# Performance work log

Hardware: AMD Instinct MI355X
Metric: run time of the kernel (lower is better)

## Reference

```python
import jax, jax.numpy as jnp
import numpy as np

D_MODEL = 1024
D_FF = 4096


def _layernorm(x, g, b, eps=1e-5):
    mu = jnp.mean(x, axis=-1, keepdims=True)
    var = jnp.var(x, axis=-1, keepdims=True)
    return (x - mu) * jax.lax.rsqrt(var + eps) * g + b


def setup_inputs() -> dict:
    key = jax.random.key(0)
    ks = jax.random.split(key, 16)
    d, f = D_MODEL, D_FF
    s = 1.0 / np.sqrt(d)
    inp = {
        'x': jax.random.normal(ks[0], (4, 2048, d), dtype=jnp.float32),
        'wq': jax.random.uniform(ks[1], (d, d), jnp.float32, -s, s),
        'bq': jax.random.uniform(ks[2], (d,), jnp.float32, -s, s),
        'wk': jax.random.uniform(ks[3], (d, d), jnp.float32, -s, s),
        'bk': jax.random.uniform(ks[4], (d,), jnp.float32, -s, s),
        'wv': jax.random.uniform(ks[5], (d, d), jnp.float32, -s, s),
        'bv': jax.random.uniform(ks[6], (d,), jnp.float32, -s, s),
        'wo': jax.random.uniform(ks[7], (d, d), jnp.float32, -s, s),
        'bo': jax.random.uniform(ks[8], (d,), jnp.float32, -s, s),
        'w1': jax.random.uniform(ks[9], (d, f), jnp.float32, -s, s),
        'b1': jax.random.uniform(ks[10], (f,), jnp.float32, -s, s),
        'w2': jax.random.uniform(ks[11], (f, d), jnp.float32, -1.0 / np.sqrt(f), 1.0 / np.sqrt(f)),
        'b2': jax.random.uniform(ks[12], (d,), jnp.float32, -1.0 / np.sqrt(f), 1.0 / np.sqrt(f)),
        'g1': jnp.ones((d,), jnp.float32),
        'be1': jnp.zeros((d,), jnp.float32),
        'g2': jnp.ones((d,), jnp.float32),
        'be2': jnp.zeros((d,), jnp.float32),
    }
    return inp


def reference(x, wq, bq, wk, bk, wv, bv, wo, bo, w1, b1, w2, b2, g1, be1, g2, be2):
    d_k = x.shape[-1]
    q = jnp.einsum('bsd,de->bse', x, wq) + bq
    k = jnp.einsum('bsd,de->bse', x, wk) + bk
    v = jnp.einsum('bsd,de->bse', x, wv) + bv
    # full-width attention (no head split in the original module)
    scores = jnp.einsum('bqd,bkd->bqk', q, k) / jnp.sqrt(jnp.float32(d_k))
    attn = jax.nn.softmax(scores, axis=-1)
    ctx = jnp.einsum('bqk,bkd->bqd', attn, v)
    attn_out = jnp.einsum('bsd,de->bse', ctx, wo) + bo
    x1 = _layernorm(x + attn_out, g1, be1)
    ff = jnp.einsum('bsf,fd->bsd', jax.nn.relu(jnp.einsum('bsd,df->bsf', x1, w1) + b1), w2) + b2
    return _layernorm(x1 + ff, g2, be2)
```

## Files before the change

kernel.cpp:

```cpp
#include <hip/hip_runtime.h>
#include <stdint.h>


using f32x4 = __attribute__((ext_vector_type(4))) float;
using s16x8 = __attribute__((ext_vector_type(8))) short;

__device__ __forceinline__ ushort f2b(float f) {
    union { float f; uint32_t u; } v; v.f = f;
    uint32_t u = v.u;
    return (ushort)((u + 0x7fffu + ((u >> 16) & 1u)) >> 16);
}
__device__ __forceinline__ float b2f(ushort b) {
    union { uint32_t u; float f; } v; v.u = ((uint32_t)b) << 16;
    return v.f;
}
__device__ __forceinline__ float to_f(float f) { return f; }
__device__ __forceinline__ float to_f(ushort b) { return b2f(b); }

__device__ __forceinline__ void async_ld16(const ushort* g, ushort* l) {
    __builtin_amdgcn_global_load_lds(
        (const __attribute__((address_space(1))) void*)g,
        (__attribute__((address_space(3))) void*)l,
        16, 0, 0);
}


__global__ __launch_bounds__(256) void cast_f2b4(const float* __restrict__ src,
                                                 ushort* __restrict__ dst,
                                                 long long n4) {
    long long i = (long long)blockIdx.x * 256 + threadIdx.x;
    if (i >= n4) return;
    float4 f = ((const float4*)src)[i];
    ushort4 o;
    o.x = f2b(f.x); o.y = f2b(f.y); o.z = f2b(f.z); o.w = f2b(f.w);
    ((ushort4*)dst)[i] = o;
}


template <typename T>
__global__ __launch_bounds__(256) void transpose_to_bf16(const T* __restrict__ src,
                                                         ushort* __restrict__ dst,
                                                         int R, int C, int srcLd,
                                                         long long ss, long long ds) {
    __shared__ float tile[32][33];
    src += (long long)blockIdx.z * ss;
    dst += (long long)blockIdx.z * ds;
    const int c0 = blockIdx.x * 32;
    const int r0 = blockIdx.y * 32;
    const int tx = threadIdx.x, ty = threadIdx.y;
#pragma unroll
    for (int i = 0; i < 4; i++) {
        int r = r0 + ty + i * 8;
        tile[ty + i * 8][tx] = to_f(src[(long long)r * srcLd + c0 + tx]);
    }
    __syncthreads();
#pragma unroll
    for (int i = 0; i < 4; i++) {
        int r = c0 + ty + i * 8;
        dst[(long long)r * R + r0 + tx] = f2b(tile[tx][ty + i * 8]);
    }
}


#define BM 128
#define BN 128
#define BKK 32

template <int OUT_BF16, int RELU, int HAS_BIAS>
__global__ __launch_bounds__(256) void gemm_bt(const ushort* __restrict__ A,
                                               const ushort* __restrict__ BT,
                                               void* __restrict__ Cp,
                                               const float* __restrict__ bias,
                                               int N, int K, int kChunks, float scale,
                                               int lda, int ldb, int ldc,
                                               long long sA, long long sB, long long sC,
                                               long long sK) {
    __shared__ ushort As[BM * BKK];
    __shared__ ushort Bs[BN * BKK];

    const int tid = threadIdx.x;
    const int kIdx = blockIdx.z % kChunks;
    const int bz = blockIdx.z / kChunks;
    const int kLen = K / kChunks;
    const int kOff = kIdx * kLen;
    const ushort* Ab = A + (long long)bz * sA;
    const ushort* Bb = BT + (long long)bz * sB;

    const int W = gridDim.x, H = gridDim.y;
    const int b = blockIdx.y * W + blockIdx.x;
    const int Hp = H >> 3;
    const int xcd = b & 7;
    const int s = b >> 3;
    const int tn = s / Hp;
    const int tm = xcd * Hp + (s % Hp);

    const int lane = tid & 63;
    const int wave = tid >> 6;
    const int wm = (wave >> 1) * 64;
    const int wn = (wave & 1) * 64;
    const int quad = lane >> 4;
    const int l16 = lane & 15;

    const int srow = wave * 32 + (lane >> 2);
    const int scol = (lane & 3) * 8;
    const ushort* AgL = Ab + (long long)(tm * BM + srow) * lda + scol + kOff;
    const ushort* BgL = Bb + (long long)(tn * BN + srow) * ldb + scol + kOff;
    ushort* AsL = As + wave * 1024;
    ushort* BsL = Bs + wave * 1024;
    const long long rstepA = (long long)16 * lda;
    const long long rstepB = (long long)16 * ldb;

    f32x4 acc[4][4];
#pragma unroll
    for (int i = 0; i < 4; i++)
#pragma unroll
        for (int j = 0; j < 4; j++) acc[i][j] = (f32x4){0.f, 0.f, 0.f, 0.f};

    for (int k0 = 0; k0 < kLen; k0 += BKK) {
        async_ld16(AgL + k0, AsL);
        async_ld16(AgL + rstepA + k0, AsL + 512);
        async_ld16(BgL + k0, BsL);
        async_ld16(BgL + rstepB + k0, BsL + 512);
        __syncthreads();

        s16x8 af[4], bf[4];
#pragma unroll
        for (int i = 0; i < 4; i++)
            af[i] = *(const s16x8*)&As[(wm + i * 16 + l16) * BKK + quad * 8];
#pragma unroll
        for (int j = 0; j < 4; j++)
            bf[j] = *(const s16x8*)&Bs[(wn + j * 16 + l16) * BKK + quad * 8];
#pragma unroll
        for (int i = 0; i < 4; i++)
#pragma unroll
            for (int j = 0; j < 4; j++)
                acc[i][j] = __builtin_amdgcn_mfma_f32_16x16x32_bf16(af[i], bf[j], acc[i][j], 0, 0, 0);
        __syncthreads();
    }

    const long long cb = (long long)bz * sC + (long long)kIdx * sK;
    float* Cf = (float*)Cp;
    ushort* Cb = (ushort*)Cp;
#pragma unroll
    for (int j = 0; j < 4; j++) {
        const int col = tn * BN + wn + j * 16 + l16;
        float bv = (HAS_BIAS && kIdx == 0) ? bias[col] : 0.0f;
#pragma unroll
        for (int i = 0; i < 4; i++) {
            const int row0 = tm * BM + wm + i * 16 + quad * 4;
#pragma unroll
            for (int r = 0; r < 4; r++) {
                float v = acc[i][j][r] * scale + bv;
                if (RELU) v = v > 0.f ? v : 0.f;
                long long idx = cb + (long long)(row0 + r) * ldc + col;
                if (OUT_BF16) Cb[idx] = f2b(v);
                else Cf[idx] = v;
            }
        }
    }
}


__global__ __launch_bounds__(256) void softmax_rows(const float* __restrict__ S,
                                                    ushort* __restrict__ P) {
    const int C = 2048;
    const long long row = blockIdx.x;
    const float* s = S + row * C;
    ushort* p = P + row * C;
    const int tid = threadIdx.x;
    float v[8];
    float mx = -1e30f;
#pragma unroll
    for (int i = 0; i < 8; i++) {
        v[i] = s[tid + i * 256];
        mx = fmaxf(mx, v[i]);
    }
    __shared__ float red[256];
    red[tid] = mx;
    __syncthreads();
    for (int off = 128; off > 0; off >>= 1) {
        if (tid < off) red[tid] = fmaxf(red[tid], red[tid + off]);
        __syncthreads();
    }
    mx = red[0];
    __syncthreads();
    float sum = 0.f;
#pragma unroll
    for (int i = 0; i < 8; i++) {
        v[i] = __expf(v[i] - mx);
        sum += v[i];
    }
    red[tid] = sum;
    __syncthreads();
    for (int off = 128; off > 0; off >>= 1) {
        if (tid < off) red[tid] += red[tid + off];
        __syncthreads();
    }
    float inv = 1.f / red[0];
#pragma unroll
    for (int i = 0; i < 8; i++) p[tid + i * 256] = f2b(v[i] * inv);
}


__global__ __launch_bounds__(256) void residual_ln(const float* __restrict__ X,
                                                   const float* __restrict__ Y,
                                                   const float* __restrict__ Y2,
                                                   const float* __restrict__ g,
                                                   const float* __restrict__ be,
                                                   float* __restrict__ outf,
                                                   ushort* __restrict__ outb) {
    const int D = 1024;
    const long long row = blockIdx.x;
    const float* x = X + row * D;
    const float* y = Y + row * D;
    const float* y2 = Y2 ? Y2 + row * D : nullptr;
    const int tid = threadIdx.x;
    float v[4];
    float s = 0.f, s2 = 0.f;
#pragma unroll
    for (int i = 0; i < 4; i++) {
        int c = tid + i * 256;
        float t = x[c] + y[c];
        if (y2) t += y2[c];
        v[i] = t;
        s += t;
        s2 += t * t;
    }
    __shared__ float r1[256], r2[256];
    r1[tid] = s;
    r2[tid] = s2;
    __syncthreads();
    for (int off = 128; off > 0; off >>= 1) {
        if (tid < off) {
            r1[tid] += r1[tid + off];
            r2[tid] += r2[tid + off];
        }
        __syncthreads();
    }
    float mu = r1[0] * (1.f / 1024.f);
    float var = r2[0] * (1.f / 1024.f) - mu * mu;
    float inv = rsqrtf(var + 1e-5f);
    float* of = outf + row * D;
    ushort* ob = outb ? outb + row * D : nullptr;
#pragma unroll
    for (int i = 0; i < 4; i++) {
        int c = tid + i * 256;
        float o = (v[i] - mu) * inv * g[c] + be[c];
        of[c] = o;
        if (ob) ob[c] = f2b(o);
    }
}


extern "C" void kernel_launch(void* const* d_in, const int* in_sizes, int n_in,
                              void* d_out, int out_size, void* d_ws, size_t ws_size,
                              hipStream_t stream) {
    const float* x  = (const float*)d_in[0];
    const float* wq = (const float*)d_in[1];
    const float* bq = (const float*)d_in[2];
    const float* wk = (const float*)d_in[3];
    const float* bk = (const float*)d_in[4];
    const float* wv = (const float*)d_in[5];
    const float* bv = (const float*)d_in[6];
    const float* wo = (const float*)d_in[7];
    const float* bo = (const float*)d_in[8];
    const float* w1 = (const float*)d_in[9];
    const float* b1 = (const float*)d_in[10];
    const float* w2 = (const float*)d_in[11];
    const float* b2 = (const float*)d_in[12];
    const float* g1 = (const float*)d_in[13];
    const float* be1 = (const float*)d_in[14];
    const float* g2 = (const float*)d_in[15];
    const float* be2 = (const float*)d_in[16];
    float* out = (float*)d_out;
    char* ws = (char*)d_ws;

    const int Bz = 4, S = 2048, D = 1024, F = 4096;
    const int T = Bz * S;
    const size_t MBy = 1024ull * 1024ull;

    ushort* qkvT = (ushort*)(ws + 0);
    ushort* woT  = (ushort*)(ws + 6 * MBy);
    ushort* w1T  = (ushort*)(ws + 8 * MBy);
    ushort* w2T  = (ushort*)(ws + 16 * MBy);
    float*  bqkv = (float*)(ws + 24 * MBy);
    ushort* xb   = (ushort*)(ws + 25 * MBy);
    ushort* qkv  = (ushort*)(ws + 41 * MBy);
    ushort* vT   = (ushort*)(ws + 89 * MBy);
    float*  sc   = (float*)(ws + 105 * MBy);
    ushort* attn = (ushort*)(ws + 169 * MBy);
    ushort* ctx = (ushort*)(ws + 25 * MBy);
    float*  ao  = (float*)(ws + 105 * MBy);
    float*  x1  = (float*)(ws + 41 * MBy);
    ushort* x1b = (ushort*)(ws + 73 * MBy);
    ushort* h   = (ushort*)(ws + 105 * MBy);
    float*  ff0 = (float*)(ws + 169 * MBy);
    float*  ff1 = (float*)(ws + 73 * MBy);

    dim3 b32(32, 8);

    cast_f2b4<<<(T * D) / 1024, 256, 0, stream>>>(x, xb, (long long)(T * D) / 4);

    transpose_to_bf16<float><<<dim3(32, 32, 1), b32, 0, stream>>>(wq, qkvT, D, D, D, 0, 0);
    transpose_to_bf16<float><<<dim3(32, 32, 1), b32, 0, stream>>>(wk, qkvT + 1024 * 1024, D, D, D, 0, 0);
    transpose_to_bf16<float><<<dim3(32, 32, 1), b32, 0, stream>>>(wv, qkvT + 2048 * 1024, D, D, D, 0, 0);
    transpose_to_bf16<float><<<dim3(32, 32, 1), b32, 0, stream>>>(wo, woT, D, D, D, 0, 0);
    transpose_to_bf16<float><<<dim3(128, 32, 1), b32, 0, stream>>>(w1, w1T, D, F, F, 0, 0);
    transpose_to_bf16<float><<<dim3(32, 128, 1), b32, 0, stream>>>(w2, w2T, F, D, D, 0, 0);

    hipMemcpyAsync(bqkv, bq, D * sizeof(float), hipMemcpyDeviceToDevice, stream);
    hipMemcpyAsync(bqkv + D, bk, D * sizeof(float), hipMemcpyDeviceToDevice, stream);
    hipMemcpyAsync(bqkv + 2 * D, bv, D * sizeof(float), hipMemcpyDeviceToDevice, stream);

    gemm_bt<1, 0, 1><<<dim3(3 * D / 128, T / 128, 1), 256, 0, stream>>>(
        xb, qkvT, qkv, bqkv, 3 * D, D, 1, 1.f, D, D, 3 * D, 0, 0, 0, 0);

    transpose_to_bf16<ushort><<<dim3(D / 32, S / 32, Bz), b32, 0, stream>>>(
        qkv + 2048, vT, S, D, 3 * D, (long long)S * 3 * D, (long long)S * D);

    gemm_bt<0, 0, 0><<<dim3(S / 128, S / 128, Bz), 256, 0, stream>>>(
        qkv, qkv + 1024, sc, nullptr, S, D, 1, 0.03125f, 3 * D, 3 * D, S,
        (long long)S * 3 * D, (long long)S * 3 * D, (long long)S * S, 0);

    softmax_rows<<<T, 256, 0, stream>>>(sc, attn);

    gemm_bt<1, 0, 0><<<dim3(D / 128, S / 128, Bz), 256, 0, stream>>>(
        attn, vT, ctx, nullptr, D, S, 1, 1.f, S, S, D,
        (long long)S * S, (long long)D * S, (long long)S * D, 0);

    gemm_bt<0, 0, 1><<<dim3(D / 128, T / 128, 1), 256, 0, stream>>>(
        ctx, woT, ao, bo, D, D, 1, 1.f, D, D, D, 0, 0, 0, 0);

    residual_ln<<<T, 256, 0, stream>>>(x, ao, nullptr, g1, be1, x1, x1b);

    gemm_bt<1, 1, 1><<<dim3(F / 128, T / 128, 1), 256, 0, stream>>>(
        x1b, w1T, h, b1, F, D, 1, 1.f, D, D, F, 0, 0, 0, 0);

    gemm_bt<0, 0, 1><<<dim3(D / 128, T / 128, 2), 256, 0, stream>>>(
        h, w2T, ff0, b2, D, F, 2, 1.f, F, F, D, 0, 0, 0, (long long)(ff1 - ff0));

    residual_ln<<<T, 256, 0, stream>>>(x1, ff0, ff1, g2, be2, out, nullptr);
}
```

Baseline: 661.1 us.

## Double-buffer GEMM LDS loads, emit bf16 scores, vectorize softmax, split-K output projection

The GEMM now double-buffers its shared-memory tiles, prefetching the next K slice with async global-to-LDS loads while MFMAs run on the current one. It uses explicit vmcnt waits and raw barriers in place of __syncthreads. The attention-score GEMM now writes bf16 instead of fp32, halving score traffic, and softmax reads and writes contiguous ushort4 vectors. The output projection is split-K in two with both partials summed in the residual layernorm. The bf16 scores cut precision before softmax, and the hand-coded waitcnt encodings could be wrong for this target.

```diff
diff --git a/kernel.cpp b/kernel.cpp
--- a/kernel.cpp
+++ b/kernel.cpp
@@ -23,6 +23,9 @@
         (__attribute__((address_space(3))) void*)l,
         16, 0, 0);
 }
+
+#define WAITCNT_VM4 0x0F74
+#define WAITCNT_VM0 0x0F70
 
 
 __global__ __launch_bounds__(256) void cast_f2b4(const float* __restrict__ src,
@@ -65,6 +68,7 @@
 #define BM 128
 #define BN 128
 #define BKK 32
+#define TILE_ELEMS (BM * BKK)
 
 template <int OUT_BF16, int RELU, int HAS_BIAS>
 __global__ __launch_bounds__(256) void gemm_bt(const ushort* __restrict__ A,
@@ -75,8 +79,8 @@
                                                int lda, int ldb, int ldc,
                                                long long sA, long long sB, long long sC,
                                                long long sK) {
-    __shared__ ushort As[BM * BKK];
-    __shared__ ushort Bs[BN * BKK];
+    __shared__ ushort As[2 * TILE_ELEMS];
+    __shared__ ushort Bs[2 * TILE_ELEMS];
 
     const int tid = threadIdx.x;
     const int kIdx = blockIdx.z % kChunks;
@@ -116,26 +120,44 @@
 #pragma unroll
         for (int j = 0; j < 4; j++) acc[i][j] = (f32x4){0.f, 0.f, 0.f, 0.f};
 
+    {
+        async_ld16(AgL, AsL);
+        async_ld16(AgL + rstepA, AsL + 512);
+        async_ld16(BgL, BsL);
+        async_ld16(BgL + rstepB, BsL + 512);
+    }
+
+    int p = 0;
     for (int k0 = 0; k0 < kLen; k0 += BKK) {
-        async_ld16(AgL + k0, AsL);
-        async_ld16(AgL + rstepA + k0, AsL + 512);
-        async_ld16(BgL + k0, BsL);
-        async_ld16(BgL + rstepB + k0, BsL + 512);
-        __syncthreads();
-
+        if (k0 + BKK < kLen) {
+            const int q = p ^ 1;
+            async_ld16(AgL + (k0 + BKK), AsL + q * TILE_ELEMS);
+            async_ld16(AgL + rstepA + (k0 + BKK), AsL + q * TILE_ELEMS + 512);
+            async_ld16(BgL + (k0 + BKK), BsL + q * TILE_ELEMS);
+            async_ld16(BgL + rstepB + (k0 + BKK), BsL + q * TILE_ELEMS + 512);
+            __builtin_amdgcn_s_waitcnt(WAITCNT_VM4);
+        } else {
+            __builtin_amdgcn_s_waitcnt(WAITCNT_VM0);
+        }
+        __builtin_amdgcn_s_barrier();
+
+        const ushort* Asp = As + p * TILE_ELEMS;
+        const ushort* Bsp = Bs + p * TILE_ELEMS;
         s16x8 af[4], bf[4];
 #pragma unroll
         for (int i = 0; i < 4; i++)
-            af[i] = *(const s16x8*)&As[(wm + i * 16 + l16) * BKK + quad * 8];
+            af[i] = *(const s16x8*)&Asp[(wm + i * 16 + l16) * BKK + quad * 8];
 #pragma unroll
         for (int j = 0; j < 4; j++)
-            bf[j] = *(const s16x8*)&Bs[(wn + j * 16 + l16) * BKK + quad * 8];
+            bf[j] = *(const s16x8*)&Bsp[(wn + j * 16 + l16) * BKK + quad * 8];
 #pragma unroll
         for (int i = 0; i < 4; i++)
 #pragma unroll
             for (int j = 0; j < 4; j++)
                 acc[i][j] = __builtin_amdgcn_mfma_f32_16x16x32_bf16(af[i], bf[j], acc[i][j], 0, 0, 0);
-        __syncthreads();
+
+        __builtin_amdgcn_s_barrier();
+        p ^= 1;
     }
 
     const long long cb = (long long)bz * sC + (long long)kIdx * sK;
@@ -161,20 +183,19 @@
 }
 
 
-__global__ __launch_bounds__(256) void softmax_rows(const float* __restrict__ S,
+__global__ __launch_bounds__(256) void softmax_rows(const ushort* __restrict__ S,
                                                     ushort* __restrict__ P) {
     const int C = 2048;
     const long long row = blockIdx.x;
-    const float* s = S + row * C;
-    ushort* p = P + row * C;
     const int tid = threadIdx.x;
+    const ushort4* s4 = (const ushort4*)(S + row * C) + tid * 2;
+    ushort4 a = s4[0], bq = s4[1];
     float v[8];
+    v[0] = b2f(a.x); v[1] = b2f(a.y); v[2] = b2f(a.z); v[3] = b2f(a.w);
+    v[4] = b2f(bq.x); v[5] = b2f(bq.y); v[6] = b2f(bq.z); v[7] = b2f(bq.w);
     float mx = -1e30f;
 #pragma unroll
-    for (int i = 0; i < 8; i++) {
-        v[i] = s[tid + i * 256];
-        mx = fmaxf(mx, v[i]);
-    }
+    for (int i = 0; i < 8; i++) mx = fmaxf(mx, v[i]);
     __shared__ float red[256];
     red[tid] = mx;
     __syncthreads();
@@ -197,8 +218,12 @@
         __syncthreads();
     }
     float inv = 1.f / red[0];
-#pragma unroll
-    for (int i = 0; i < 8; i++) p[tid + i * 256] = f2b(v[i] * inv);
+    ushort4 o0, o1;
+    o0.x = f2b(v[0] * inv); o0.y = f2b(v[1] * inv); o0.z = f2b(v[2] * inv); o0.w = f2b(v[3] * inv);
+    o1.x = f2b(v[4] * inv); o1.y = f2b(v[5] * inv); o1.z = f2b(v[6] * inv); o1.w = f2b(v[7] * inv);
+    ushort4* p4 = (ushort4*)(P + row * C) + tid * 2;
+    p4[0] = o0;
+    p4[1] = o1;
 }
 
 
@@ -287,10 +312,11 @@
     ushort* xb   = (ushort*)(ws + 25 * MBy);
     ushort* qkv  = (ushort*)(ws + 41 * MBy);
     ushort* vT   = (ushort*)(ws + 89 * MBy);
-    float*  sc   = (float*)(ws + 105 * MBy);
+    ushort* scb  = (ushort*)(ws + 105 * MBy);
     ushort* attn = (ushort*)(ws + 169 * MBy);
     ushort* ctx = (ushort*)(ws + 25 * MBy);
-    float*  ao  = (float*)(ws + 105 * MBy);
+    float*  ao0 = (float*)(ws + 105 * MBy);
+    float*  ao1 = (float*)(ws + 137 * MBy);
     float*  x1  = (float*)(ws + 41 * MBy);
     ushort* x1b = (ushort*)(ws + 73 * MBy);
     ushort* h   = (ushort*)(ws + 105 * MBy);
@@ -318,20 +344,20 @@
     transpose_to_bf16<ushort><<<dim3(D / 32, S / 32, Bz), b32, 0, stream>>>(
         qkv + 2048, vT, S, D, 3 * D, (long long)S * 3 * D, (long long)S * D);
 
-    gemm_bt<0, 0, 0><<<dim3(S / 128, S / 128, Bz), 256, 0, stream>>>(
-        qkv, qkv + 1024, sc, nullptr, S, D, 1, 0.03125f, 3 * D, 3 * D, S,
+    gemm_bt<1, 0, 0><<<dim3(S / 128, S / 128, Bz), 256, 0, stream>>>(
+        qkv, qkv + 1024, scb, nullptr, S, D, 1, 0.03125f, 3 * D, 3 * D, S,
         (long long)S * 3 * D, (long long)S * 3 * D, (long long)S * S, 0);
 
-    softmax_rows<<<T, 256, 0, stream>>>(sc, attn);
+    softmax_rows<<<T, 256, 0, stream>>>(scb, attn);
 
     gemm_bt<1, 0, 0><<<dim3(D / 128, S / 128, Bz), 256, 0, stream>>>(
         attn, vT, ctx, nullptr, D, S, 1, 1.f, S, S, D,
         (long long)S * S, (long long)D * S, (long long)S * D, 0);
 
-    gemm_bt<0, 0, 1><<<dim3(D / 128, T / 128, 1), 256, 0, stream>>>(
-        ctx, woT, ao, bo, D, D, 1, 1.f, D, D, D, 0, 0, 0, 0);
-
-    residual_ln<<<T, 256, 0, stream>>>(x, ao, nullptr, g1, be1, x1, x1b);
+    gemm_bt<0, 0, 1><<<dim3(D / 128, T / 128, 2), 256, 0, stream>>>(
+        ctx, woT, ao0, bo, D, D, 2, 1.f, D, D, D, 0, 0, 0, (long long)(ao1 - ao0));
+
+    residual_ln<<<T, 256, 0, stream>>>(x, ao0, ao1, g1, be1, x1, x1b);
 
     gemm_bt<1, 1, 1><<<dim3(F / 128, T / 128, 1), 256, 0, stream>>>(
         x1b, w1T, h, b1, F, D, 1, 1.f, D, D, F, 0, 0, 0, 0);
```

Measured after the change: 630.5 us. 1.05x faster.
